# Kernel tuning notes

Measured on AMD Instinct MI355X. Metric: run time of the kernel, lower is better.

## Reference

```python
import jax, jax.numpy as jnp
import numpy as np

IMG = 128                  # img_size
FMM = 35.0
SENSOR = 32.0
FUV = FMM * IMG / SENSOR   # focal length in pixels (screen space, in_ndc=False)
N_PTS = 16384
CHUNK = 1024               # points per scan step
R_SIL = 0.008              # silhouette pass radius (NDC)
R_DEP = 0.012              # depth pass radius (NDC)
K_SIL = 8
K_DEP = 16
DIST = 1.2


def _look_at(dist, elev_deg, azim_deg):
    # PyTorch3D look_at_view_transform with at=origin, up=+Y, degrees=True
    elev = jnp.deg2rad(elev_deg)
    azim = jnp.deg2rad(azim_deg)
    cam = jnp.stack([dist * jnp.cos(elev) * jnp.sin(azim),
                     dist * jnp.sin(elev),
                     dist * jnp.cos(elev) * jnp.cos(azim)], axis=-1)  # (B,3)
    up = jnp.array([0.0, 1.0, 0.0], dtype=cam.dtype)
    z_ax = -cam / (jnp.linalg.norm(cam, axis=-1, keepdims=True) + 1e-8)
    x_ax = jnp.cross(jnp.broadcast_to(up, z_ax.shape), z_ax)
    x_ax = x_ax / (jnp.linalg.norm(x_ax, axis=-1, keepdims=True) + 1e-8)
    y_ax = jnp.cross(z_ax, x_ax)
    R = jnp.stack([x_ax, y_ax, z_ax], axis=-1)   # columns are camera axes
    T = -jnp.einsum('bi,bij->bj', cam, R)        # X_cam = X_world @ R + T
    return R, T


def _project(pts, R, T):
    # world -> camera (row-vector convention) -> screen px -> PyTorch3D NDC
    Xc = jnp.einsum('bni,bij->bnj', pts, R) + T[:, None, :]
    z = Xc[..., 2]
    z_safe = jnp.where(z > 1e-5, z, 1.0)  # points behind camera are culled anyway
    xs = FUV * Xc[..., 0] / z_safe + IMG / 2.0
    ys = FUV * Xc[..., 1] / z_safe + IMG / 2.0
    x_ndc = 1.0 - 2.0 * xs / IMG
    y_ndc = 1.0 - 2.0 * ys / IMG
    return jnp.stack([x_ndc, y_ndc], axis=-1), z


def _rasterize(xy, z, r2, K):
    """Per-pixel K nearest-in-depth points within per-point NDC radius.
    xy: (B,N,2) NDC, z: (B,N) camera depth, r2: (B,N) squared radius.
    Returns zbuf, dists of shape (B,IMG,IMG,K), -1 for empty slots."""
    B, N, _ = xy.shape
    P = IMG * IMG
    # pixel-center NDC grid (PyTorch3D: +X left, +Y up; row-major flatten)
    gxs = 1.0 - (2.0 * jnp.arange(IMG, dtype=xy.dtype) + 1.0) / IMG  # per column
    gys = 1.0 - (2.0 * jnp.arange(IMG, dtype=xy.dtype) + 1.0) / IMG  # per row
    gx = jnp.tile(gxs, IMG)          # (P,)
    gy = jnp.repeat(gys, IMG)        # (P,)

    nch = N // CHUNK
    px = xy[..., 0].reshape(B, nch, CHUNK).swapaxes(0, 1)
    py = xy[..., 1].reshape(B, nch, CHUNK).swapaxes(0, 1)
    pz = z.reshape(B, nch, CHUNK).swapaxes(0, 1)
    pr2 = r2.reshape(B, nch, CHUNK).swapaxes(0, 1)

    def body(carry, c):
        top_z, top_d = carry
        cx, cy, cz, cr2 = c                               # each (B,CHUNK)
        dx = gx[None, :, None] - cx[:, None, :]           # (B,P,CHUNK)
        dy = gy[None, :, None] - cy[:, None, :]
        d2 = dx * dx + dy * dy
        ok = (d2 < cr2[:, None, :]) & (cz[:, None, :] > 0.0)
        zc = jnp.where(ok, cz[:, None, :], jnp.inf)
        cand_z = jnp.concatenate([top_z, zc], axis=-1)    # (B,P,K+CHUNK)
        cand_d = jnp.concatenate([top_d, d2], axis=-1)
        negz, idx = jax.lax.top_k(-cand_z, K)             # K smallest depths
        return (-negz, jnp.take_along_axis(cand_d, idx, axis=-1)), None

    init = (jnp.full((B, P, K), jnp.inf, dtype=xy.dtype),
            jnp.zeros((B, P, K), dtype=xy.dtype))
    (top_z, top_d), _ = jax.lax.scan(jax.checkpoint(body), init, (px, py, pz, pr2))
    valid = jnp.isfinite(top_z)
    zbuf = jnp.where(valid, top_z, -1.0).reshape(B, IMG, IMG, K)
    dists = jnp.where(valid, top_d, -1.0).reshape(B, IMG, IMG, K)
    return zbuf, dists


def setup_inputs() -> dict:
    key = jax.random.key(0)
    k1, k2 = jax.random.split(key)
    point_cloud = jax.random.normal(k1, (2, N_PTS, 6), dtype=jnp.float32) * 0.25
    param = jax.random.normal(k2, (2, 8, 3), dtype=jnp.float32) * 20.0  # degrees
    return {"point_cloud": point_cloud, "param": param}


def reference(point_cloud, param):
    pts = point_cloud[..., :3]
    B = pts.shape[0]
    elev0 = param[:, 1, 0]
    azim0 = param[:, 0, 0]

    # ---- silhouette pass (radius 0.008, K=8) + alpha compositing ----
    R0, T0 = _look_at(DIST, elev0, azim0)
    xy0, z0 = _project(pts, R0, T0)
    r2_sil = jnp.full((B, N_PTS), R_SIL * R_SIL, dtype=pts.dtype)
    _, dists_s = _rasterize(xy0, z0, r2_sil, K_SIL)
    alphas = jnp.where(dists_s >= 0.0, 1.0 - dists_s / (R_SIL * R_SIL), 0.0)
    trans = jnp.cumprod(1.0 - alphas, axis=-1)
    trans_excl = jnp.concatenate([jnp.ones_like(trans[..., :1]), trans[..., :-1]], axis=-1)
    sihlt_map = jnp.sum(alphas * trans_excl, axis=-1, keepdims=True) * 255.0  # (B,H,W,1)

    # ---- depth pass with random view (radius 0.012, K=16) ----
    kd = jax.random.key(42)
    ke, ka = jax.random.split(kd)
    elev_d = jax.random.uniform(ke, (B,), dtype=pts.dtype) * 60.0 - 30.0
    azim_d = jax.random.uniform(ka, (B,), dtype=pts.dtype) * 300.0 + azim0 + 30.0
    Rd, Td = _look_at(DIST, elev_d, azim_d)
    xyd, zd = _project(pts, Rd, Td)
    r2_dep = jnp.full((B, N_PTS), R_DEP * R_DEP, dtype=pts.dtype)
    zbuf_d, _ = _rasterize(xyd, zd, r2_dep, K_DEP)
    depth_ini = zbuf_d[..., 0]

    # density-aware adaptive radius (detached, per source .detach())
    area = jnp.sum((jax.lax.stop_gradient(depth_ini) > 0.0).astype(pts.dtype), axis=(1, 2))
    pa_radius = area / 16384.0 * 0.057                      # (B,)
    r2_ada = jnp.broadcast_to((pa_radius * pa_radius)[:, None], (B, N_PTS))

    zbuf_a, dists_a = _rasterize(xyd, zd, r2_ada, K_DEP)
    depth_img = zbuf_a[..., :8]
    dist_top = dists_a[..., :8]
    return (sihlt_map, depth_img, dist_top)
```

## Files before the change

kernel.cpp:

```cpp
#include <hip/hip_runtime.h>
#include <hip/hip_cooperative_groups.h>
#include <cstring>
#include <cstdint>

namespace cg = cooperative_groups;

#define NPTS 16384
#define FUVC 140.0f
#define R_SILF 0.008f
#define R_DEPF 0.012f
#define R2_SIL (0.008f*0.008f)
#define R2_DEP (0.012f*0.012f)
#define CH 512

#define AREA_OFF  48
#define PA_OFF    50
#define R2ADA_OFF 52
#define CNT_SIL   64
#define OFF_SIL   2112
#define CNT_ADA   4160
#define OFF_ADA   6208
#define FLAGS8    8256
#define FLAGS     8256
#define ZERO_END  16448
#define PROJ0     41024
#define PROJ1     172096
#define LSILF     303168
#define LADAF     827456
#define WS1_WORDS 2007104u
#define WS1_NEEDED ((size_t)WS1_WORDS * 4u)
#define LSIL      303168
#define LADA      434240
#define WS2_WORDS 729152u
#define WS2_NEEDED ((size_t)WS2_WORDS * 4u)

#define FUSED_BLOCKS 1024
#define FUSED_NT (FUSED_BLOCKS * 256)

__device__ __forceinline__ void cam_calc(float elev, float azim, float c[12]) {
    const float D2R = 0.017453292519943295f;
    float er = elev * D2R, ar = azim * D2R;
    float ce = cosf(er), se = sinf(er), ca = cosf(ar), sa = sinf(ar);
    float cx = 1.2f * ce * sa, cy = 1.2f * se, cz = 1.2f * ce * ca;
    float n = sqrtf(cx*cx + cy*cy + cz*cz) + 1e-8f;
    float zx = -cx / n, zy = -cy / n, zz = -cz / n;
    float xx = zz, xy = 0.0f, xz = -zx;
    float xn = sqrtf(xx*xx + xy*xy + xz*xz) + 1e-8f;
    xx /= xn; xz /= xn;
    float yx = zy*xz - zz*xy, yy = zz*xx - zx*xz, yz = zx*xy - zy*xx;
    c[0]=xx; c[1]=xy; c[2]=xz; c[3]=yx; c[4]=yy; c[5]=yz;
    c[6]=zx; c[7]=zy; c[8]=zz;
    c[9]  = -(cx*xx + cy*xy + cz*xz);
    c[10] = -(cx*yx + cy*yy + cz*yz);
    c[11] = -(cx*zx + cy*zy + cz*zz);
}

__device__ __forceinline__ void cam_compute(const float* __restrict__ param,
                                            float* __restrict__ ws,
                                            int t, float ue0, float ue1,
                                            float ua0, float ua1) {
    int b = t >> 1, cam = t & 1;
    float azim0 = param[b * 24 + 0];
    float elev0 = param[b * 24 + 3];
    float elev, azim;
    if (cam == 0) { elev = elev0; azim = azim0; }
    else {
        float ue = b ? ue1 : ue0;
        float ua = b ? ua1 : ua0;
        elev = ue * 60.0f - 30.0f;
        azim = ua * 300.0f + azim0 + 30.0f;
    }
    float c[12];
    cam_calc(elev, azim, c);
    float* w = ws + t * 12;
    #pragma unroll
    for (int i = 0; i < 12; i++) w[i] = c[i];
}

__device__ __forceinline__ float4 project_pt(const float* __restrict__ P,
                                             const float c[12]) {
    float X = P[0], Y = P[1], Z = P[2];
    float xc = X*c[0] + Y*c[1] + Z*c[2] + c[9];
    float yc = X*c[3] + Y*c[4] + Z*c[5] + c[10];
    float zc = X*c[6] + Y*c[7] + Z*c[8] + c[11];
    float zs = zc > 1e-5f ? zc : 1.0f;
    float px = 1.0f - (FUVC * xc / zs + 64.0f) * (1.0f/64.0f);
    float py = 1.0f - (FUVC * yc / zs + 64.0f) * (1.0f/64.0f);
    return make_float4(px, py, zc, 0.0f);
}

__device__ __forceinline__ void pix_range(float p, float r, int& lo, int& hi) {
    float lo_f = (1.0f - p - r) * 64.0f - 0.5f;
    float hi_f = (1.0f - p + r) * 64.0f - 0.5f;
    lo = (int)ceilf(lo_f - 1e-3f);
    hi = (int)floorf(hi_f + 1e-3f);
    lo = max(lo, 0); hi = min(hi, 127);
}

__device__ __forceinline__ void top8_insert(float z, float d,
                                            float tz[8], float td[8]) {
    #pragma unroll
    for (int k = 0; k < 8; k++) {
        bool lt = z < tz[k];
        float oz = tz[k], od = td[k];
        if (lt) { tz[k] = z; td[k] = d; z = oz; d = od; }
    }
}

__device__ __forceinline__ void hit_test(float4 pt, float gx, float gy, float r2,
                                         float tz[8], float td[8]) {
    float dx = gx - pt.x, dy = gy - pt.y;
    float d2 = dx*dx + dy*dy;
    if (d2 < r2 && pt.z > 0.0f && pt.z < tz[7]) top8_insert(pt.z, d2, tz, td);
}

__device__ __forceinline__ void merge_sorted8(float tz[8], float td[8], int mask) {
    float oz[8], od[8];
    #pragma unroll
    for (int k = 0; k < 8; k++) {
        oz[k] = __shfl_xor(tz[k], mask);
        od[k] = __shfl_xor(td[k], mask);
    }
    float mz[8], md[8];
    #pragma unroll
    for (int k = 0; k < 8; k++) {
        bool take = oz[7 - k] < tz[k];
        mz[k] = take ? oz[7 - k] : tz[k];
        md[k] = take ? od[7 - k] : td[k];
    }
    #define CE(i, j) { bool sw = mz[j] < mz[i]; \
        float t1 = mz[i], t2 = md[i]; \
        mz[i] = sw ? mz[j] : mz[i]; md[i] = sw ? md[j] : md[i]; \
        mz[j] = sw ? t1 : mz[j];    md[j] = sw ? t2 : md[j]; }
    CE(0,4) CE(1,5) CE(2,6) CE(3,7)
    CE(0,2) CE(1,3) CE(4,6) CE(5,7)
    CE(0,1) CE(2,3) CE(4,5) CE(6,7)
    #undef CE
    #pragma unroll
    for (int k = 0; k < 8; k++) { tz[k] = mz[k]; td[k] = md[k]; }
}

__device__ __forceinline__ void scan1024(unsigned* uw, unsigned cbase,
                                         unsigned obase, unsigned* s, int t) {
    unsigned c0 = uw[cbase + t*4 + 0];
    unsigned c1 = uw[cbase + t*4 + 1];
    unsigned c2 = uw[cbase + t*4 + 2];
    unsigned c3 = uw[cbase + t*4 + 3];
    unsigned tot = c0 + c1 + c2 + c3;
    s[t] = tot; __syncthreads();
    for (int off = 1; off < 256; off <<= 1) {
        unsigned v = (t >= off) ? s[t - off] : 0u;
        __syncthreads();
        s[t] += v;
        __syncthreads();
    }
    unsigned base = s[t] - tot;
    uw[obase + t*4 + 0] = base;
    uw[obase + t*4 + 1] = base + c0;
    uw[obase + t*4 + 2] = base + c0 + c1;
    uw[obase + t*4 + 3] = base + c0 + c1 + c2;
    uw[cbase + t*4 + 0] = 0;
    uw[cbase + t*4 + 1] = 0;
    uw[cbase + t*4 + 2] = 0;
    uw[cbase + t*4 + 3] = 0;
}

__device__ __forceinline__ void body_proj(const float* __restrict__ pc,
                                          float* __restrict__ ws, int b, int p) {
    unsigned* uw = (unsigned*)ws;
    unsigned char* fb = (unsigned char*)(uw + FLAGS8);
    const float* P = pc + ((size_t)b * NPTS + p) * 6;
    float c0[12], c1[12];
    const float* w0 = ws + (b * 2) * 12;
    #pragma unroll
    for (int i = 0; i < 12; i++) { c0[i] = w0[i]; c1[i] = w0[12 + i]; }

    float4 q0 = project_pt(P, c0);
    ((float4*)(ws + PROJ0))[b * NPTS + p] = q0;
    if (q0.z > 0.0f) {
        int cl, chh, rl, rh;
        pix_range(q0.x, R_SILF, cl, chh);
        pix_range(q0.y, R_SILF, rl, rh);
        if (cl <= chh && rl <= rh) {
            int bxl = cl >> 2, bxh = chh >> 2, byl = rl >> 2, byh = rh >> 2;
            for (int by = byl; by <= byh; by++)
                for (int bx = bxl; bx <= bxh; bx++)
                    atomicAdd(&uw[CNT_SIL + b * 1024 + by * 32 + bx], 1u);
        }
    }

    float4 q1 = project_pt(P, c1);
    ((float4*)(ws + PROJ1))[b * NPTS + p] = q1;
    if (q1.z > 0.0f) {
        int cl, chh, rl, rh;
        pix_range(q1.x, R_DEPF, cl, chh);
        pix_range(q1.y, R_DEPF, rl, rh);
        for (int rr = rl; rr <= rh; rr++) {
            float gy = 1.0f - (float)(2 * rr + 1) * (1.0f/128.0f);
            float dy = gy - q1.y;
            for (int cc = cl; cc <= chh; cc++) {
                float gx = 1.0f - (float)(2 * cc + 1) * (1.0f/128.0f);
                float dx = gx - q1.x;
                float d2 = dx*dx + dy*dy;
                if (d2 < R2_DEP) fb[b * NPTS + rr * 128 + cc] = 1;
            }
        }
    }
}

__device__ __forceinline__ void body_area_scan(float* __restrict__ ws, int job,
                                               int t, unsigned* s) {
    unsigned* uw = (unsigned*)ws;
    if (job < 2) {
        int b = job;
        unsigned acc = 0;
        #pragma unroll
        for (int j = 0; j < 16; j++) {
            unsigned w = uw[FLAGS8 + b * 4096 + t * 16 + j];
            acc += __popc(w & 0x01010101u);
        }
        s[t] = acc; __syncthreads();
        for (int off = 128; off > 0; off >>= 1) {
            if (t < off) s[t] += s[t + off];
            __syncthreads();
        }
        if (t == 0) {
            unsigned area = s[0];
            uw[AREA_OFF + b] = area;
            float pa = (float)area * (1.0f/16384.0f) * 0.057f;
            ws[PA_OFF + b] = pa;
            ws[R2ADA_OFF + b] = pa * pa;
        }
    } else {
        int b = job - 2;
        scan1024(uw, CNT_SIL + b * 1024, OFF_SIL + b * 1024, s, t);
    }
}

__device__ __forceinline__ void body_cnt_ada(float* __restrict__ ws, int p) {
    unsigned* uw = (unsigned*)ws;
    int b = p >> 14;
    float4 q = ((const float4*)(ws + PROJ1))[p];
    float pa = ws[PA_OFF + b];
    if (q.z > 0.0f) {
        int cl, chh, rl, rh;
        pix_range(q.x, pa, cl, chh);
        pix_range(q.y, pa, rl, rh);
        if (cl <= chh && rl <= rh) {
            int bxl = cl >> 2, bxh = chh >> 2, byl = rl >> 2, byh = rh >> 2;
            for (int by = byl; by <= byh; by++)
                for (int bx = bxl; bx <= bxh; bx++)
                    atomicAdd(&uw[CNT_ADA + b * 1024 + by * 32 + bx], 1u);
        }
    }
}

__device__ __forceinline__ void body_scat_sil(float* __restrict__ ws, int p) {
    unsigned* uw = (unsigned*)ws;
    int b = p >> 14;
    float4 q = ((const float4*)(ws + PROJ0))[p];
    if (q.z > 0.0f) {
        int cl, chh, rl, rh;
        pix_range(q.x, R_SILF, cl, chh);
        pix_range(q.y, R_SILF, rl, rh);
        if (cl <= chh && rl <= rh) {
            int bxl = cl >> 2, bxh = chh >> 2, byl = rl >> 2, byh = rh >> 2;
            for (int by = byl; by <= byh; by++)
                for (int bx = bxl; bx <= bxh; bx++) {
                    unsigned bin = b * 1024 + by * 32 + bx;
                    unsigned idx = uw[OFF_SIL + bin] + atomicAdd(&uw[CNT_SIL + bin], 1u);
                    ((float4*)(ws + LSILF))[b * 65536 + idx] = q;
                }
        }
    }
}

__device__ __forceinline__ void body_scan_ada(float* __restrict__ ws, int b, int t) {
    unsigned* uw = (unsigned*)ws;
    unsigned c[16]; unsigned tot = 0;
    #pragma unroll
    for (int j = 0; j < 16; j++) { c[j] = uw[CNT_ADA + b * 1024 + t * 16 + j]; tot += c[j]; }
    unsigned inc = tot;
    #pragma unroll
    for (int off = 1; off < 64; off <<= 1) {
        unsigned v = __shfl_up(inc, off);
        if (t >= off) inc += v;
    }
    unsigned base = inc - tot;
    #pragma unroll
    for (int j = 0; j < 16; j++) {
        uw[OFF_ADA + b * 1024 + t * 16 + j] = base;
        base += c[j];
        uw[CNT_ADA + b * 1024 + t * 16 + j] = 0u;
    }
}

__device__ __forceinline__ void body_scat_ada(float* __restrict__ ws, int p) {
    unsigned* uw = (unsigned*)ws;
    int b = p >> 14;
    float4 q = ((const float4*)(ws + PROJ1))[p];
    float pa = ws[PA_OFF + b];
    if (q.z > 0.0f) {
        int cl, chh, rl, rh;
        pix_range(q.x, pa, cl, chh);
        pix_range(q.y, pa, rl, rh);
        if (cl <= chh && rl <= rh) {
            int bxl = cl >> 2, bxh = chh >> 2, byl = rl >> 2, byh = rh >> 2;
            for (int by = byl; by <= byh; by++)
                for (int bx = bxl; bx <= bxh; bx++) {
                    unsigned bin = b * 1024 + by * 32 + bx;
                    unsigned idx = uw[OFF_ADA + bin] + atomicAdd(&uw[CNT_ADA + bin], 1u);
                    ((float4*)(ws + LADAF))[b * 147456 + idx] = q;
                }
        }
    }
}

__device__ __forceinline__ void body_gather(const float* __restrict__ ws,
                                            float* __restrict__ out,
                                            int id, int lane) {
    const unsigned* uw = (const unsigned*)ws;
    bool sil = id < 2048;
    int gt = sil ? id : id - 2048;
    int b = gt >> 10;
    int tile = gt & 1023;
    int p = lane & 15, s = lane >> 4;
    int bx = tile & 31, by = tile >> 5;
    int col = (bx << 2) + (p & 3), row = (by << 2) + (p >> 2);
    float gx = 1.0f - (float)(2*col + 1) * (1.0f/128.0f);
    float gy = 1.0f - (float)(2*row + 1) * (1.0f/128.0f);
    float r2 = sil ? R2_SIL : ws[R2ADA_OFF + b];
    unsigned start = sil ? uw[OFF_SIL + b * 1024 + tile] : uw[OFF_ADA + b * 1024 + tile];
    unsigned len   = sil ? uw[CNT_SIL + b * 1024 + tile] : uw[CNT_ADA + b * 1024 + tile];
    const float4* lst = sil ? ((const float4*)(ws + LSILF)) + b * 65536 + start
                            : ((const float4*)(ws + LADAF)) + b * 147456 + start;

    float tz[8], td[8];
    #pragma unroll
    for (int k = 0; k < 8; k++) { tz[k] = INFINITY; td[k] = 0.0f; }

    unsigned i = (unsigned)s;
    while (i + 28 < len) {
        float4 cb[8];
        #pragma unroll
        for (int u = 0; u < 8; u++) cb[u] = lst[i + 4u * (unsigned)u];
        #pragma unroll
        for (int u = 0; u < 8; u++) hit_test(cb[u], gx, gy, r2, tz, td);
        i += 32;
    }
    for (; i < len; i += 4) hit_test(lst[i], gx, gy, r2, tz, td);

    merge_sorted8(tz, td, 16);
    merge_sorted8(tz, td, 32);

    if (s == 0) {
        int pix = (b << 14) + row * 128 + col;
        if (sil) {
            float trans = 1.0f, acc = 0.0f;
            #pragma unroll
            for (int k = 0; k < 8; k++) {
                float a = (tz[k] != INFINITY) ? (1.0f - td[k] / R2_SIL) : 0.0f;
                acc += a * trans;
                trans *= (1.0f - a);
            }
            out[pix] = acc * 255.0f;
        } else {
            float* dep = out + 32768  + (size_t)pix * 8;
            float* dst = out + 294912 + (size_t)pix * 8;
            #pragma unroll
            for (int k = 0; k < 8; k++) {
                bool v = (tz[k] != INFINITY);
                dep[k] = v ? tz[k] : -1.0f;
                dst[k] = v ? td[k] : -1.0f;
            }
        }
    }
}

__global__ __launch_bounds__(256) void k_fused(const float* __restrict__ pc,
                                               const float* __restrict__ param,
                                               float* __restrict__ ws,
                                               float* __restrict__ out,
                                               float ue0, float ue1,
                                               float ua0, float ua1) {
    cg::grid_group grid = cg::this_grid();
    unsigned* uw = (unsigned*)ws;
    __shared__ unsigned s[256];
    int tid = blockIdx.x * 256 + threadIdx.x;

    for (int i = 48 + tid; i < ZERO_END; i += FUSED_NT) uw[i] = 0u;
    if (tid < 4) cam_compute(param, ws, tid, ue0, ue1, ua0, ua1);
    grid.sync();

    if (tid < 2 * NPTS) body_proj(pc, ws, tid >> 14, tid & (NPTS - 1));
    grid.sync();

    if (blockIdx.x < 4) body_area_scan(ws, blockIdx.x, threadIdx.x, s);
    grid.sync();

    if (tid < 2 * NPTS) body_cnt_ada(ws, tid);
    else if (tid < 4 * NPTS) body_scat_sil(ws, tid - 2 * NPTS);
    grid.sync();

    if (blockIdx.x == 0 && threadIdx.x < 128)
        body_scan_ada(ws, threadIdx.x >> 6, threadIdx.x & 63);
    grid.sync();

    if (tid < 2 * NPTS) body_scat_ada(ws, tid);
    grid.sync();

    body_gather(ws, out, tid >> 6, tid & 63);
}


__global__ __launch_bounds__(256) void k_zero(float* __restrict__ ws) {
    unsigned* uw = (unsigned*)ws;
    int gid = blockIdx.x * 256 + threadIdx.x;
    int stride = gridDim.x * 256;
    for (int i = gid; i < ZERO_END; i += stride) uw[i] = 0u;
}

__global__ __launch_bounds__(256) void k_proj_v3(const float* __restrict__ pc,
                                                 const float* __restrict__ param,
                                                 float* __restrict__ ws,
                                                 float ue0, float ue1,
                                                 float ua0, float ua1) {
    int b = blockIdx.x >> 6;
    int p = ((blockIdx.x & 63) << 8) + threadIdx.x;
    float azim0 = param[b * 24 + 0];
    float elev0 = param[b * 24 + 3];
    float c0[12], c1[12];
    cam_calc(elev0, azim0, c0);
    float ue = b ? ue1 : ue0;
    float ua = b ? ua1 : ua0;
    cam_calc(ue * 60.0f - 30.0f, ua * 300.0f + azim0 + 30.0f, c1);

    unsigned* uw = (unsigned*)ws;
    unsigned char* fb = (unsigned char*)(uw + FLAGS8);
    const float* P = pc + ((size_t)b * NPTS + p) * 6;

    float4 q0 = project_pt(P, c0);
    ((float4*)(ws + PROJ0))[b * NPTS + p] = q0;
    if (q0.z > 0.0f) {
        int cl, chh, rl, rh;
        pix_range(q0.x, R_SILF, cl, chh);
        pix_range(q0.y, R_SILF, rl, rh);
        if (cl <= chh && rl <= rh) {
            int bxl = cl >> 2, bxh = chh >> 2, byl = rl >> 2, byh = rh >> 2;
            for (int by = byl; by <= byh; by++)
                for (int bx = bxl; bx <= bxh; bx++)
                    atomicAdd(&uw[CNT_SIL + b * 1024 + by * 32 + bx], 1u);
        }
    }
    float4 q1 = project_pt(P, c1);
    ((float4*)(ws + PROJ1))[b * NPTS + p] = q1;
    if (q1.z > 0.0f) {
        int cl, chh, rl, rh;
        pix_range(q1.x, R_DEPF, cl, chh);
        pix_range(q1.y, R_DEPF, rl, rh);
        for (int rr = rl; rr <= rh; rr++) {
            float gy = 1.0f - (float)(2 * rr + 1) * (1.0f/128.0f);
            float dy = gy - q1.y;
            for (int cc = cl; cc <= chh; cc++) {
                float gx = 1.0f - (float)(2 * cc + 1) * (1.0f/128.0f);
                float dx = gx - q1.x;
                float d2 = dx*dx + dy*dy;
                if (d2 < R2_DEP) fb[b * NPTS + rr * 128 + cc] = 1;
            }
        }
    }
}

__global__ __launch_bounds__(256) void k_area_scan_v3(float* __restrict__ ws) {
    __shared__ unsigned s[256];
    body_area_scan(ws, blockIdx.x, threadIdx.x, s);
}

__global__ __launch_bounds__(64) void k_cntada_scatsil(float* __restrict__ ws) {
    int id = blockIdx.x;
    bool isCnt = id < 512;
    int p = ((isCnt ? id : id - 512) << 6) + threadIdx.x;
    if (isCnt) body_cnt_ada(ws, p);
    else       body_scat_sil(ws, p);
}

__global__ __launch_bounds__(64) void k_scan_ada64(float* __restrict__ ws) {
    body_scan_ada(ws, blockIdx.x, threadIdx.x);
}

__global__ __launch_bounds__(64) void k_scatter_ada_v2(float* __restrict__ ws) {
    body_scat_ada(ws, (blockIdx.x << 6) + threadIdx.x);
}

__global__ __launch_bounds__(64) void k_gather_v3(const float* __restrict__ ws,
                                                  float* __restrict__ out) {
    body_gather(ws, out, blockIdx.x, threadIdx.x);
}


__global__ __launch_bounds__(256) void k_init(const float* __restrict__ param,
                                              float* __restrict__ ws,
                                              float ue0, float ue1,
                                              float ua0, float ua1) {
    unsigned* uw = (unsigned*)ws;
    int gid = blockIdx.x * 256 + threadIdx.x;
    int stride = gridDim.x * 256;
    for (int i = gid; i < 2048; i += stride) { uw[CNT_SIL + i] = 0u; uw[CNT_ADA + i] = 0u; }
    for (int i = gid; i < 32768; i += stride) uw[FLAGS + i] = 0u;
    if (gid < 2) uw[AREA_OFF + gid] = 0u;
    if (gid < 4) cam_compute(param, ws, gid, ue0, ue1, ua0, ua1);
}

__global__ __launch_bounds__(256) void k_proj_count(const float* __restrict__ pc,
                                                    float* __restrict__ ws) {
    unsigned* uw = (unsigned*)ws;
    int b = blockIdx.x >> 6;
    int p = ((blockIdx.x & 63) << 8) + threadIdx.x;
    const float* P = pc + ((size_t)b * NPTS + p) * 6;
    float c0[12], c1[12];
    const float* w0 = ws + (b * 2) * 12;
    #pragma unroll
    for (int i = 0; i < 12; i++) { c0[i] = w0[i]; c1[i] = w0[12 + i]; }

    float4 q0 = project_pt(P, c0);
    ((float4*)(ws + PROJ0))[b * NPTS + p] = q0;
    if (q0.z > 0.0f) {
        int cl, chh, rl, rh;
        pix_range(q0.x, R_SILF, cl, chh);
        pix_range(q0.y, R_SILF, rl, rh);
        if (cl <= chh && rl <= rh) {
            int bxl = cl >> 2, bxh = chh >> 2, byl = rl >> 2, byh = rh >> 2;
            for (int by = byl; by <= byh; by++)
                for (int bx = bxl; bx <= bxh; bx++)
                    atomicAdd(&uw[CNT_SIL + b * 1024 + by * 32 + bx], 1u);
        }
    }
    float4 q1 = project_pt(P, c1);
    ((float4*)(ws + PROJ1))[b * NPTS + p] = q1;
    if (q1.z > 0.0f) {
        int cl, chh, rl, rh;
        pix_range(q1.x, R_DEPF, cl, chh);
        pix_range(q1.y, R_DEPF, rl, rh);
        for (int rr = rl; rr <= rh; rr++) {
            float gy = 1.0f - (float)(2 * rr + 1) * (1.0f/128.0f);
            float dy = gy - q1.y;
            for (int cc = cl; cc <= chh; cc++) {
                float gx = 1.0f - (float)(2 * cc + 1) * (1.0f/128.0f);
                float dx = gx - q1.x;
                float d2 = dx*dx + dy*dy;
                if (d2 < R2_DEP) uw[FLAGS + b * NPTS + rr * 128 + cc] = 1u;
            }
        }
    }
}

__global__ __launch_bounds__(256) void k_area_scan(float* __restrict__ ws) {
    unsigned* uw = (unsigned*)ws;
    __shared__ unsigned s[256];
    int t = threadIdx.x;
    int job = blockIdx.x;
    if (job < 2) {
        int b = job;
        unsigned acc = 0;
        for (int i = t; i < NPTS; i += 256) acc += uw[FLAGS + b * NPTS + i];
        s[t] = acc; __syncthreads();
        for (int off = 128; off > 0; off >>= 1) {
            if (t < off) s[t] += s[t + off];
            __syncthreads();
        }
        if (t == 0) {
            unsigned area = s[0];
            uw[AREA_OFF + b] = area;
            float pa = (float)area * (1.0f/16384.0f) * 0.057f;
            ws[PA_OFF + b] = pa;
            ws[R2ADA_OFF + b] = pa * pa;
        }
    } else {
        int b = job - 2;
        scan1024(uw, CNT_SIL + b * 1024, OFF_SIL + b * 1024, s, t);
    }
}

__global__ __launch_bounds__(256) void k_count_ada(float* __restrict__ ws) {
    unsigned* uw = (unsigned*)ws;
    int b = blockIdx.x >> 6;
    int p = ((blockIdx.x & 63) << 8) + threadIdx.x;
    float4 q = ((const float4*)(ws + PROJ1))[b * NPTS + p];
    float pa = ws[PA_OFF + b];
    if (q.z > 0.0f) {
        int cl, chh, rl, rh;
        pix_range(q.x, pa, cl, chh);
        pix_range(q.y, pa, rl, rh);
        if (cl <= chh && rl <= rh) {
            int bxl = cl >> 2, bxh = chh >> 2, byl = rl >> 2, byh = rh >> 2;
            for (int by = byl; by <= byh; by++)
                for (int bx = bxl; bx <= bxh; bx++)
                    atomicAdd(&uw[CNT_ADA + b * 1024 + by * 32 + bx], 1u);
        }
    }
}

__global__ __launch_bounds__(256) void k_scan_ada(float* __restrict__ ws) {
    unsigned* uw = (unsigned*)ws;
    __shared__ unsigned s[256];
    int b = blockIdx.x;
    scan1024(uw, CNT_ADA + b * 1024, OFF_ADA + b * 1024, s, threadIdx.x);
}

__global__ __launch_bounds__(256) void k_scatter(float* __restrict__ ws) {
    unsigned* uw = (unsigned*)ws;
    int b = blockIdx.x >> 6;
    int p = ((blockIdx.x & 63) << 8) + threadIdx.x;

    float4 q0 = ((const float4*)(ws + PROJ0))[b * NPTS + p];
    if (q0.z > 0.0f) {
        int cl, chh, rl, rh;
        pix_range(q0.x, R_SILF, cl, chh);
        pix_range(q0.y, R_SILF, rl, rh);
        if (cl <= chh && rl <= rh) {
            int bxl = cl >> 2, bxh = chh >> 2, byl = rl >> 2, byh = rh >> 2;
            for (int by = byl; by <= byh; by++)
                for (int bx = bxl; bx <= bxh; bx++) {
                    unsigned bin = b * 1024 + by * 32 + bx;
                    unsigned idx = uw[OFF_SIL + bin] + atomicAdd(&uw[CNT_SIL + bin], 1u);
                    uw[LSIL + b * 65536 + idx] = (unsigned)p;
                }
        }
    }
    float4 q1 = ((const float4*)(ws + PROJ1))[b * NPTS + p];
    float pa = ws[PA_OFF + b];
    if (q1.z > 0.0f) {
        int cl, chh, rl, rh;
        pix_range(q1.x, pa, cl, chh);
        pix_range(q1.y, pa, rl, rh);
        if (cl <= chh && rl <= rh) {
            int bxl = cl >> 2, bxh = chh >> 2, byl = rl >> 2, byh = rh >> 2;
            for (int by = byl; by <= byh; by++)
                for (int bx = bxl; bx <= bxh; bx++) {
                    unsigned bin = b * 1024 + by * 32 + bx;
                    unsigned idx = uw[OFF_ADA + bin] + atomicAdd(&uw[CNT_ADA + bin], 1u);
                    uw[LADA + b * 147456 + idx] = (unsigned)p;
                }
        }
    }
}

__global__ __launch_bounds__(256) void k_gather_sil(const float* __restrict__ ws,
                                                    float* __restrict__ out) {
    const unsigned* uw = (const unsigned*)ws;
    int b = blockIdx.x >> 6;
    int tile = (blockIdx.x & 63) * 16 + (threadIdx.x >> 4);
    int q = threadIdx.x & 15;
    int bx = tile & 31, by = tile >> 5;
    int col = (bx << 2) + (q & 3), row = (by << 2) + (q >> 2);
    float gx = 1.0f - (float)(2*col + 1) * (1.0f/128.0f);
    float gy = 1.0f - (float)(2*row + 1) * (1.0f/128.0f);
    unsigned start = uw[OFF_SIL + b * 1024 + tile];
    unsigned len   = uw[CNT_SIL + b * 1024 + tile];
    const float4* pr = (const float4*)(ws + PROJ0) + b * NPTS;

    float tz[8], td[8];
    #pragma unroll
    for (int k = 0; k < 8; k++) { tz[k] = INFINITY; td[k] = 0.0f; }
    for (unsigned i = 0; i < len; i++) {
        unsigned pid = uw[LSIL + b * 65536 + start + i];
        hit_test(pr[pid], gx, gy, R2_SIL, tz, td);
    }
    float trans = 1.0f, s = 0.0f;
    #pragma unroll
    for (int k = 0; k < 8; k++) {
        float a = (tz[k] != INFINITY) ? (1.0f - td[k] / R2_SIL) : 0.0f;
        s += a * trans;
        trans *= (1.0f - a);
    }
    out[(b << 14) + row * 128 + col] = s * 255.0f;
}

__global__ __launch_bounds__(256) void k_gather_ada(const float* __restrict__ ws,
                                                    float* __restrict__ out) {
    const unsigned* uw = (const unsigned*)ws;
    int b = blockIdx.x >> 6;
    int tile = (blockIdx.x & 63) * 16 + (threadIdx.x >> 4);
    int q = threadIdx.x & 15;
    int bx = tile & 31, by = tile >> 5;
    int col = (bx << 2) + (q & 3), row = (by << 2) + (q >> 2);
    float gx = 1.0f - (float)(2*col + 1) * (1.0f/128.0f);
    float gy = 1.0f - (float)(2*row + 1) * (1.0f/128.0f);
    float r2 = ws[R2ADA_OFF + b];
    unsigned start = uw[OFF_ADA + b * 1024 + tile];
    unsigned len   = uw[CNT_ADA + b * 1024 + tile];
    const float4* pr = (const float4*)(ws + PROJ1) + b * NPTS;

    float tz[8], td[8];
    #pragma unroll
    for (int k = 0; k < 8; k++) { tz[k] = INFINITY; td[k] = 0.0f; }
    for (unsigned i = 0; i < len; i++) {
        unsigned pid = uw[LADA + b * 147456 + start + i];
        hit_test(pr[pid], gx, gy, r2, tz, td);
    }
    int pix = (b << 14) + row * 128 + col;
    float* dep = out + 32768  + (size_t)pix * 8;
    float* dst = out + 294912 + (size_t)pix * 8;
    #pragma unroll
    for (int k = 0; k < 8; k++) {
        bool v = (tz[k] != INFINITY);
        dep[k] = v ? tz[k] : -1.0f;
        dst[k] = v ? td[k] : -1.0f;
    }
}

__global__ void cam_kernel_fb(const float* __restrict__ param, float* __restrict__ ws,
                              float ue0, float ue1, float ua0, float ua1) {
    int t = threadIdx.x;
    if (t < 2) ws[48 + t] = 0.0f;
    if (t >= 4) return;
    cam_compute(param, ws, t, ue0, ue1, ua0, ua1);
}

__device__ __forceinline__ void stage_points(const float* __restrict__ pcb,
                                             const float c[12], int c0, float4* sp) {
    for (int i = threadIdx.x; i < CH; i += 256) {
        const float* P = pcb + (size_t)(c0 + i) * 6;
        sp[i] = project_pt(P, c);
    }
}

__global__ __launch_bounds__(256) void raster_AB(const float* __restrict__ pc,
                                                 float* __restrict__ ws,
                                                 float* __restrict__ out) {
    __shared__ float4 sp[CH];
    int bid = blockIdx.x;
    bool silMode = bid < 128;
    int q = silMode ? bid : bid - 128;
    int b = q >> 6;
    int p = ((q & 63) << 8) + threadIdx.x;
    const float* cw = ws + (b * 2 + (silMode ? 0 : 1)) * 12;
    float c[12];
    #pragma unroll
    for (int i = 0; i < 12; i++) c[i] = cw[i];
    float r2 = silMode ? R2_SIL : R2_DEP;
    int col = p & 127, row = p >> 7;
    float gx = 1.0f - (float)(2*col + 1) * (1.0f/128.0f);
    float gy = 1.0f - (float)(2*row + 1) * (1.0f/128.0f);
    const float* pcb = pc + (size_t)b * NPTS * 6;

    if (silMode) {
        float tz[8], td[8];
        #pragma unroll
        for (int k = 0; k < 8; k++) { tz[k] = INFINITY; td[k] = 0.0f; }
        for (int c0 = 0; c0 < NPTS; c0 += CH) {
            __syncthreads();
            stage_points(pcb, c, c0, sp);
            __syncthreads();
            #pragma unroll 4
            for (int j = 0; j < CH; j++) hit_test(sp[j], gx, gy, r2, tz, td);
        }
        float trans = 1.0f, s = 0.0f;
        #pragma unroll
        for (int k = 0; k < 8; k++) {
            float a = (tz[k] != INFINITY) ? (1.0f - td[k] / r2) : 0.0f;
            s += a * trans;
            trans *= (1.0f - a);
        }
        out[(b << 14) + p] = s * 255.0f;
    } else {
        float mz = INFINITY;
        for (int c0 = 0; c0 < NPTS; c0 += CH) {
            __syncthreads();
            stage_points(pcb, c, c0, sp);
            __syncthreads();
            #pragma unroll 4
            for (int j = 0; j < CH; j++) {
                float4 pt = sp[j];
                float dx = gx - pt.x, dy = gy - pt.y;
                float d2 = dx*dx + dy*dy;
                if (d2 < r2 && pt.z > 0.0f) mz = fminf(mz, pt.z);
            }
        }
        unsigned long long m = __ballot(mz != INFINITY);
        if ((threadIdx.x & 63) == 0)
            atomicAdd(ws + 48 + b, (float)__popcll(m));
    }
}

__global__ __launch_bounds__(256) void raster_C(const float* __restrict__ pc,
                                                const float* __restrict__ ws,
                                                float* __restrict__ out) {
    __shared__ float4 sp[CH];
    int bid = blockIdx.x;
    int b = bid >> 6;
    int p = ((bid & 63) << 8) + threadIdx.x;
    const float* cw = ws + (b * 2 + 1) * 12;
    float c[12];
    #pragma unroll
    for (int i = 0; i < 12; i++) c[i] = cw[i];
    float area = ws[48 + b];
    float pa = (area * (1.0f/16384.0f)) * 0.057f;
    float r2 = pa * pa;
    int col = p & 127, row = p >> 7;
    float gx = 1.0f - (float)(2*col + 1) * (1.0f/128.0f);
    float gy = 1.0f - (float)(2*row + 1) * (1.0f/128.0f);
    const float* pcb = pc + (size_t)b * NPTS * 6;

    float tz[8], td[8];
    #pragma unroll
    for (int k = 0; k < 8; k++) { tz[k] = INFINITY; td[k] = 0.0f; }
    for (int c0 = 0; c0 < NPTS; c0 += CH) {
        __syncthreads();
        stage_points(pcb, c, c0, sp);
        __syncthreads();
        #pragma unroll 4
        for (int j = 0; j < CH; j++) hit_test(sp[j], gx, gy, r2, tz, td);
    }
    float* dep = out + 32768  + (size_t)((b << 14) + p) * 8;
    float* dst = out + 294912 + (size_t)((b << 14) + p) * 8;
    #pragma unroll
    for (int k = 0; k < 8; k++) {
        bool v = (tz[k] != INFINITY);
        dep[k] = v ? tz[k] : -1.0f;
        dst[k] = v ? td[k] : -1.0f;
    }
}

static inline uint32_t rotl32(uint32_t x, int r) { return (x << r) | (x >> (32 - r)); }

static void tf2x32(uint32_t k0, uint32_t k1, uint32_t c0, uint32_t c1,
                   uint32_t* o0, uint32_t* o1) {
    uint32_t ks0 = k0, ks1 = k1, ks2 = k0 ^ k1 ^ 0x1BD11BDAu;
    uint32_t x0 = c0 + ks0, x1 = c1 + ks1;
    static const int rA[4] = {13, 15, 26, 6};
    static const int rB[4] = {17, 29, 16, 24};
    #define RND4(R) do { for (int i = 0; i < 4; i++) { x0 += x1; x1 = rotl32(x1, R[i]); x1 ^= x0; } } while (0)
    RND4(rA); x0 += ks1; x1 += ks2 + 1u;
    RND4(rB); x0 += ks2; x1 += ks0 + 2u;
    RND4(rA); x0 += ks0; x1 += ks1 + 3u;
    RND4(rB); x0 += ks1; x1 += ks2 + 4u;
    RND4(rA); x0 += ks2; x1 += ks0 + 5u;
    #undef RND4
    *o0 = x0; *o1 = x1;
}

static inline float bits_to_unit_float(uint32_t bits) {
    uint32_t fb = (bits >> 9) | 0x3f800000u;
    float f;
    memcpy(&f, &fb, 4);
    return f - 1.0f;
}

extern "C" void kernel_launch(void* const* d_in, const int* in_sizes, int n_in,
                              void* d_out, int out_size, void* d_ws, size_t ws_size,
                              hipStream_t stream) {
    const float* pc    = (const float*)d_in[0];
    const float* param = (const float*)d_in[1];
    float* out = (float*)d_out;
    float* ws  = (float*)d_ws;

    uint32_t ke0, ke1, ka0, ka1, b1, b2;
    tf2x32(0u, 42u, 0u, 0u, &ke0, &ke1);
    tf2x32(0u, 42u, 0u, 1u, &ka0, &ka1);
    float ue[2], ua[2];
    for (uint32_t i = 0; i < 2; i++) {
        tf2x32(ke0, ke1, 0u, i, &b1, &b2);
        ue[i] = bits_to_unit_float(b1 ^ b2);
        tf2x32(ka0, ka1, 0u, i, &b1, &b2);
        ua[i] = bits_to_unit_float(b1 ^ b2);
    }
    float ue0 = ue[0], ue1 = ue[1], ua0 = ua[0], ua1 = ua[1];

    if (ws_size >= WS1_NEEDED) {
        int dev = 0;
        hipGetDevice(&dev);
        hipDeviceProp_t prop;
        bool coop = (hipGetDeviceProperties(&prop, dev) == hipSuccess) &&
                    prop.cooperativeLaunch;
        if (coop) {
            int maxB = 0;
            if (hipOccupancyMaxActiveBlocksPerMultiprocessor(&maxB, k_fused, 256, 0)
                    != hipSuccess ||
                maxB * prop.multiProcessorCount < FUSED_BLOCKS)
                coop = false;
        }
        if (coop) {
            void* args[] = { (void*)&pc, (void*)&param, (void*)&ws, (void*)&out,
                             (void*)&ue0, (void*)&ue1, (void*)&ua0, (void*)&ua1 };
            hipError_t e = hipLaunchCooperativeKernel((const void*)k_fused,
                                                      dim3(FUSED_BLOCKS), dim3(256),
                                                      args, 0, stream);
            if (e == hipSuccess) return;
        }
        k_zero          <<<16, 256, 0, stream>>>(ws);
        k_proj_v3       <<<128, 256, 0, stream>>>(pc, param, ws, ue0, ue1, ua0, ua1);
        k_area_scan_v3  <<<4, 256, 0, stream>>>(ws);
        k_cntada_scatsil<<<1024, 64, 0, stream>>>(ws);
        k_scan_ada64    <<<2, 64, 0, stream>>>(ws);
        k_scatter_ada_v2<<<512, 64, 0, stream>>>(ws);
        k_gather_v3     <<<4096, 64, 0, stream>>>(ws, out);
    } else if (ws_size >= WS2_NEEDED) {
        k_init      <<<64, 256, 0, stream>>>(param, ws, ue0, ue1, ua0, ua1);
        k_proj_count<<<128, 256, 0, stream>>>(pc, ws);
        k_area_scan <<<4, 256, 0, stream>>>(ws);
        k_count_ada <<<128, 256, 0, stream>>>(ws);
        k_scan_ada  <<<2, 256, 0, stream>>>(ws);
        k_scatter   <<<128, 256, 0, stream>>>(ws);
        k_gather_sil<<<128, 256, 0, stream>>>(ws, out);
        k_gather_ada<<<128, 256, 0, stream>>>(ws, out);
    } else {
        cam_kernel_fb<<<1, 64, 0, stream>>>(param, ws, ue0, ue1, ua0, ua1);
        raster_AB<<<256, 256, 0, stream>>>(pc, ws, out);
        raster_C <<<128, 256, 0, stream>>>(pc, ws, out);
    }
}
```

Baseline: 92.22 us.

## Cut grid syncs via last-block tickets and aggregate bin atomics in shared memory

The cooperative fused kernel drops two of its grid-wide barriers. Small serial steps (area/scan, ada scan) now run in whichever block finishes last, detected with a global atomic ticket counter. Each block first builds its per-bin counts and scatter offsets in a shared-memory histogram and then issues one global atomic per bin, instead of one global atomic per point per bin. This lowers global atomic contention and barrier latency, but adds extra __syncthreads, threadfences and shared-memory work, and changes the scatter order within a bin.

Measured after the change: 92.52 us. No clear change (+0.3%).

```diff
diff --git a/kernel.cpp b/kernel.cpp
--- a/kernel.cpp
+++ b/kernel.cpp
@@ -16,6 +16,8 @@
 #define AREA_OFF  48
 #define PA_OFF    50
 #define R2ADA_OFF 52
+#define TICK0     54
+#define TICK1     55
 #define CNT_SIL   64
 #define OFF_SIL   2112
 #define CNT_ADA   4160
@@ -97,6 +99,19 @@
     lo = max(lo, 0); hi = min(hi, 127);
 }
 
+__device__ __forceinline__ void bin_bbox(float4 q, float r, int& bxl, int& bxh,
+                                         int& byl, int& byh) {
+    bxl = 0; bxh = -1; byl = 0; byh = -1;
+    if (q.z > 0.0f) {
+        int cl, chh, rl, rh;
+        pix_range(q.x, r, cl, chh);
+        pix_range(q.y, r, rl, rh);
+        if (cl <= chh && rl <= rh) {
+            bxl = cl >> 2; bxh = chh >> 2; byl = rl >> 2; byh = rh >> 2;
+        }
+    }
+}
+
 __device__ __forceinline__ void top8_insert(float z, float d,
                                             float tz[8], float td[8]) {
     #pragma unroll
@@ -165,49 +180,6 @@
     uw[cbase + t*4 + 3] = 0;
 }
 
-__device__ __forceinline__ void body_proj(const float* __restrict__ pc,
-                                          float* __restrict__ ws, int b, int p) {
-    unsigned* uw = (unsigned*)ws;
-    unsigned char* fb = (unsigned char*)(uw + FLAGS8);
-    const float* P = pc + ((size_t)b * NPTS + p) * 6;
-    float c0[12], c1[12];
-    const float* w0 = ws + (b * 2) * 12;
-    #pragma unroll
-    for (int i = 0; i < 12; i++) { c0[i] = w0[i]; c1[i] = w0[12 + i]; }
-
-    float4 q0 = project_pt(P, c0);
-    ((float4*)(ws + PROJ0))[b * NPTS + p] = q0;
-    if (q0.z > 0.0f) {
-        int cl, chh, rl, rh;
-        pix_range(q0.x, R_SILF, cl, chh);
-        pix_range(q0.y, R_SILF, rl, rh);
-        if (cl <= chh && rl <= rh) {
-            int bxl = cl >> 2, bxh = chh >> 2, byl = rl >> 2, byh = rh >> 2;
-            for (int by = byl; by <= byh; by++)
-                for (int bx = bxl; bx <= bxh; bx++)
-                    atomicAdd(&uw[CNT_SIL + b * 1024 + by * 32 + bx], 1u);
-        }
-    }
-
-    float4 q1 = project_pt(P, c1);
-    ((float4*)(ws + PROJ1))[b * NPTS + p] = q1;
-    if (q1.z > 0.0f) {
-        int cl, chh, rl, rh;
-        pix_range(q1.x, R_DEPF, cl, chh);
-        pix_range(q1.y, R_DEPF, rl, rh);
-        for (int rr = rl; rr <= rh; rr++) {
-            float gy = 1.0f - (float)(2 * rr + 1) * (1.0f/128.0f);
-            float dy = gy - q1.y;
-            for (int cc = cl; cc <= chh; cc++) {
-                float gx = 1.0f - (float)(2 * cc + 1) * (1.0f/128.0f);
-                float dx = gx - q1.x;
-                float d2 = dx*dx + dy*dy;
-                if (d2 < R2_DEP) fb[b * NPTS + rr * 128 + cc] = 1;
-            }
-        }
-    }
-}
-
 __device__ __forceinline__ void body_area_scan(float* __restrict__ ws, int job,
                                                int t, unsigned* s) {
     unsigned* uw = (unsigned*)ws;
@@ -242,37 +214,25 @@
     int b = p >> 14;
     float4 q = ((const float4*)(ws + PROJ1))[p];
     float pa = ws[PA_OFF + b];
-    if (q.z > 0.0f) {
-        int cl, chh, rl, rh;
-        pix_range(q.x, pa, cl, chh);
-        pix_range(q.y, pa, rl, rh);
-        if (cl <= chh && rl <= rh) {
-            int bxl = cl >> 2, bxh = chh >> 2, byl = rl >> 2, byh = rh >> 2;
-            for (int by = byl; by <= byh; by++)
-                for (int bx = bxl; bx <= bxh; bx++)
-                    atomicAdd(&uw[CNT_ADA + b * 1024 + by * 32 + bx], 1u);
-        }
-    }
+    int bxl, bxh, byl, byh;
+    bin_bbox(q, pa, bxl, bxh, byl, byh);
+    for (int by = byl; by <= byh; by++)
+        for (int bx = bxl; bx <= bxh; bx++)
+            atomicAdd(&uw[CNT_ADA + b * 1024 + by * 32 + bx], 1u);
 }
 
 __device__ __forceinline__ void body_scat_sil(float* __restrict__ ws, int p) {
     unsigned* uw = (unsigned*)ws;
     int b = p >> 14;
     float4 q = ((const float4*)(ws + PROJ0))[p];
-    if (q.z > 0.0f) {
-        int cl, chh, rl, rh;
-        pix_range(q.x, R_SILF, cl, chh);
-        pix_range(q.y, R_SILF, rl, rh);
-        if (cl <= chh && rl <= rh) {
-            int bxl = cl >> 2, bxh = chh >> 2, byl = rl >> 2, byh = rh >> 2;
-            for (int by = byl; by <= byh; by++)
-                for (int bx = bxl; bx <= bxh; bx++) {
-                    unsigned bin = b * 1024 + by * 32 + bx;
-                    unsigned idx = uw[OFF_SIL + bin] + atomicAdd(&uw[CNT_SIL + bin], 1u);
-                    ((float4*)(ws + LSILF))[b * 65536 + idx] = q;
-                }
-        }
-    }
+    int bxl, bxh, byl, byh;
+    bin_bbox(q, R_SILF, bxl, bxh, byl, byh);
+    for (int by = byl; by <= byh; by++)
+        for (int bx = bxl; bx <= bxh; bx++) {
+            unsigned bin = b * 1024 + by * 32 + bx;
+            unsigned idx = uw[OFF_SIL + bin] + atomicAdd(&uw[CNT_SIL + bin], 1u);
+            ((float4*)(ws + LSILF))[b * 65536 + idx] = q;
+        }
 }
 
 __device__ __forceinline__ void body_scan_ada(float* __restrict__ ws, int b, int t) {
@@ -300,20 +260,14 @@
     int b = p >> 14;
     float4 q = ((const float4*)(ws + PROJ1))[p];
     float pa = ws[PA_OFF + b];
-    if (q.z > 0.0f) {
-        int cl, chh, rl, rh;
-        pix_range(q.x, pa, cl, chh);
-        pix_range(q.y, pa, rl, rh);
-        if (cl <= chh && rl <= rh) {
-            int bxl = cl >> 2, bxh = chh >> 2, byl = rl >> 2, byh = rh >> 2;
-            for (int by = byl; by <= byh; by++)
-                for (int bx = bxl; bx <= bxh; bx++) {
-                    unsigned bin = b * 1024 + by * 32 + bx;
-                    unsigned idx = uw[OFF_ADA + bin] + atomicAdd(&uw[CNT_ADA + bin], 1u);
-                    ((float4*)(ws + LADAF))[b * 147456 + idx] = q;
-                }
-        }
-    }
+    int bxl, bxh, byl, byh;
+    bin_bbox(q, pa, bxl, bxh, byl, byh);
+    for (int by = byl; by <= byh; by++)
+        for (int bx = bxl; bx <= bxh; bx++) {
+            unsigned bin = b * 1024 + by * 32 + bx;
+            unsigned idx = uw[OFF_ADA + bin] + atomicAdd(&uw[CNT_ADA + bin], 1u);
+            ((float4*)(ws + LADAF))[b * 147456 + idx] = q;
+        }
 }
 
 __device__ __forceinline__ void body_gather(const float* __restrict__ ws,
@@ -377,36 +331,175 @@
     }
 }
 
-__global__ __launch_bounds__(256) void k_fused(const float* __restrict__ pc,
-                                               const float* __restrict__ param,
-                                               float* __restrict__ ws,
-                                               float* __restrict__ out,
-                                               float ue0, float ue1,
-                                               float ua0, float ua1) {
+__global__ __launch_bounds__(256) void k_fusedp(const float* __restrict__ pc,
+                                                const float* __restrict__ param,
+                                                float* __restrict__ ws,
+                                                float* __restrict__ out,
+                                                float ue0, float ue1,
+                                                float ua0, float ua1) {
     cg::grid_group grid = cg::this_grid();
     unsigned* uw = (unsigned*)ws;
-    __shared__ unsigned s[256];
-    int tid = blockIdx.x * 256 + threadIdx.x;
+    __shared__ unsigned sh[2048];
+    __shared__ unsigned shLast;
+    int t = threadIdx.x;
+    int tid = blockIdx.x * 256 + t;
 
     for (int i = 48 + tid; i < ZERO_END; i += FUSED_NT) uw[i] = 0u;
     if (tid < 4) cam_compute(param, ws, tid, ue0, ue1, ua0, ua1);
     grid.sync();
 
-    if (tid < 2 * NPTS) body_proj(pc, ws, tid >> 14, tid & (NPTS - 1));
+    if (blockIdx.x < 128) {
+        int b = blockIdx.x >> 6;
+        int p = ((blockIdx.x & 63) << 8) + t;
+        unsigned char* fb = (unsigned char*)(uw + FLAGS8);
+        const float* P = pc + ((size_t)b * NPTS + p) * 6;
+        float c0[12], c1[12];
+        const float* w0 = ws + (b * 2) * 12;
+        #pragma unroll
+        for (int i = 0; i < 12; i++) { c0[i] = w0[i]; c1[i] = w0[12 + i]; }
+
+        #pragma unroll
+        for (int j = 0; j < 4; j++) sh[t * 4 + j] = 0u;
+        __syncthreads();
+
+        float4 q0 = project_pt(P, c0);
+        ((float4*)(ws + PROJ0))[b * NPTS + p] = q0;
+        int bxl, bxh, byl, byh;
+        bin_bbox(q0, R_SILF, bxl, bxh, byl, byh);
+        for (int by = byl; by <= byh; by++)
+            for (int bx = bxl; bx <= bxh; bx++)
+                atomicAdd(&sh[by * 32 + bx], 1u);
+
+        float4 q1 = project_pt(P, c1);
+        ((float4*)(ws + PROJ1))[b * NPTS + p] = q1;
+        if (q1.z > 0.0f) {
+            int cl, chh, rl, rh;
+            pix_range(q1.x, R_DEPF, cl, chh);
+            pix_range(q1.y, R_DEPF, rl, rh);
+            for (int rr = rl; rr <= rh; rr++) {
+                float gyv = 1.0f - (float)(2 * rr + 1) * (1.0f/128.0f);
+                float dy = gyv - q1.y;
+                for (int cc = cl; cc <= chh; cc++) {
+                    float gxv = 1.0f - (float)(2 * cc + 1) * (1.0f/128.0f);
+                    float dx = gxv - q1.x;
+                    if (dx*dx + dy*dy < R2_DEP) fb[b * NPTS + rr * 128 + cc] = 1;
+                }
+            }
+        }
+        __syncthreads();
+        #pragma unroll
+        for (int j = 0; j < 4; j++) {
+            unsigned c = sh[t * 4 + j];
+            if (c) atomicAdd(&uw[CNT_SIL + b * 1024 + t * 4 + j], c);
+        }
+        __threadfence();
+    }
+    if (t == 0) shLast = (atomicAdd(&uw[TICK0], 1u) == FUSED_BLOCKS - 1) ? 1u : 0u;
+    __syncthreads();
+    if (shLast) {
+        __threadfence();
+        for (int job = 0; job < 4; job++) {
+            body_area_scan(ws, job, t, sh);
+            __syncthreads();
+        }
+        __threadfence();
+    }
     grid.sync();
 
-    if (blockIdx.x < 4) body_area_scan(ws, blockIdx.x, threadIdx.x, s);
+    if (blockIdx.x < 128) {
+        int b = blockIdx.x >> 6;
+        int p = ((blockIdx.x & 63) << 8) + t;
+        float4 q = ((const float4*)(ws + PROJ1))[b * NPTS + p];
+        float pa = ws[PA_OFF + b];
+        #pragma unroll
+        for (int j = 0; j < 4; j++) sh[t * 4 + j] = 0u;
+        __syncthreads();
+        int bxl, bxh, byl, byh;
+        bin_bbox(q, pa, bxl, bxh, byl, byh);
+        for (int by = byl; by <= byh; by++)
+            for (int bx = bxl; bx <= bxh; bx++)
+                atomicAdd(&sh[by * 32 + bx], 1u);
+        __syncthreads();
+        #pragma unroll
+        for (int j = 0; j < 4; j++) {
+            unsigned c = sh[t * 4 + j];
+            if (c) atomicAdd(&uw[CNT_ADA + b * 1024 + t * 4 + j], c);
+        }
+        __threadfence();
+    } else if (blockIdx.x < 256) {
+        int blk = blockIdx.x - 128;
+        int b = blk >> 6;
+        int p = ((blk & 63) << 8) + t;
+        float4 q = ((const float4*)(ws + PROJ0))[b * NPTS + p];
+        int bxl, bxh, byl, byh;
+        bin_bbox(q, R_SILF, bxl, bxh, byl, byh);
+        #pragma unroll
+        for (int j = 0; j < 4; j++) sh[t * 4 + j] = 0u;
+        __syncthreads();
+        for (int by = byl; by <= byh; by++)
+            for (int bx = bxl; bx <= bxh; bx++)
+                atomicAdd(&sh[by * 32 + bx], 1u);
+        __syncthreads();
+        #pragma unroll
+        for (int j = 0; j < 4; j++) {
+            int bin = t * 4 + j;
+            unsigned c = sh[bin];
+            unsigned gb = 0;
+            if (c) gb = uw[OFF_SIL + b * 1024 + bin] +
+                        atomicAdd(&uw[CNT_SIL + b * 1024 + bin], c);
+            sh[1024 + bin] = gb;
+            sh[bin] = 0u;
+        }
+        __syncthreads();
+        for (int by = byl; by <= byh; by++)
+            for (int bx = bxl; bx <= bxh; bx++) {
+                int bin = by * 32 + bx;
+                unsigned loc = atomicAdd(&sh[bin], 1u);
+                ((float4*)(ws + LSILF))[b * 65536 + sh[1024 + bin] + loc] = q;
+            }
+        __threadfence();
+    }
+    if (t == 0) shLast = (atomicAdd(&uw[TICK1], 1u) == FUSED_BLOCKS - 1) ? 1u : 0u;
+    __syncthreads();
+    if (shLast) {
+        __threadfence();
+        if (t < 128) body_scan_ada(ws, t >> 6, t & 63);
+        __threadfence();
+    }
     grid.sync();
 
-    if (tid < 2 * NPTS) body_cnt_ada(ws, tid);
-    else if (tid < 4 * NPTS) body_scat_sil(ws, tid - 2 * NPTS);
-    grid.sync();
-
-    if (blockIdx.x == 0 && threadIdx.x < 128)
-        body_scan_ada(ws, threadIdx.x >> 6, threadIdx.x & 63);
-    grid.sync();
-
-    if (tid < 2 * NPTS) body_scat_ada(ws, tid);
+    if (blockIdx.x < 128) {
+        int b = blockIdx.x >> 6;
+        int p = ((blockIdx.x & 63) << 8) + t;
+        float4 q = ((const float4*)(ws + PROJ1))[b * NPTS + p];
+        float pa = ws[PA_OFF + b];
+        int bxl, bxh, byl, byh;
+        bin_bbox(q, pa, bxl, bxh, byl, byh);
+        #pragma unroll
+        for (int j = 0; j < 4; j++) sh[t * 4 + j] = 0u;
+        __syncthreads();
+        for (int by = byl; by <= byh; by++)
+            for (int bx = bxl; bx <= bxh; bx++)
+                atomicAdd(&sh[by * 32 + bx], 1u);
+        __syncthreads();
+        #pragma unroll
+        for (int j = 0; j < 4; j++) {
+            int bin = t * 4 + j;
+            unsigned c = sh[bin];
+            unsigned gb = 0;
+            if (c) gb = uw[OFF_ADA + b * 1024 + bin] +
+                        atomicAdd(&uw[CNT_ADA + b * 1024 + bin], c);
+            sh[1024 + bin] = gb;
+            sh[bin] = 0u;
+        }
+        __syncthreads();
+        for (int by = byl; by <= byh; by++)
+            for (int bx = bxl; bx <= bxh; bx++) {
+                int bin = by * 32 + bx;
+                unsigned loc = atomicAdd(&sh[bin], 1u);
+                ((float4*)(ws + LADAF))[b * 147456 + sh[1024 + bin] + loc] = q;
+            }
+    }
     grid.sync();
 
     body_gather(ws, out, tid >> 6, tid & 63);
@@ -417,7 +510,7 @@
     unsigned* uw = (unsigned*)ws;
     int gid = blockIdx.x * 256 + threadIdx.x;
     int stride = gridDim.x * 256;
-    for (int i = gid; i < ZERO_END; i += stride) uw[i] = 0u;
+    for (int i = 48 + gid; i < ZERO_END; i += stride) uw[i] = 0u;
 }
 
 __global__ __launch_bounds__(256) void k_proj_v3(const float* __restrict__ pc,
@@ -441,17 +534,12 @@
 
     float4 q0 = project_pt(P, c0);
     ((float4*)(ws + PROJ0))[b * NPTS + p] = q0;
-    if (q0.z > 0.0f) {
-        int cl, chh, rl, rh;
-        pix_range(q0.x, R_SILF, cl, chh);
-        pix_range(q0.y, R_SILF, rl, rh);
-        if (cl <= chh && rl <= rh) {
-            int bxl = cl >> 2, bxh = chh >> 2, byl = rl >> 2, byh = rh >> 2;
-            for (int by = byl; by <= byh; by++)
-                for (int bx = bxl; bx <= bxh; bx++)
-                    atomicAdd(&uw[CNT_SIL + b * 1024 + by * 32 + bx], 1u);
-        }
-    }
+    int bxl, bxh, byl, byh;
+    bin_bbox(q0, R_SILF, bxl, bxh, byl, byh);
+    for (int by = byl; by <= byh; by++)
+        for (int bx = bxl; bx <= bxh; bx++)
+            atomicAdd(&uw[CNT_SIL + b * 1024 + by * 32 + bx], 1u);
+
     float4 q1 = project_pt(P, c1);
     ((float4*)(ws + PROJ1))[b * NPTS + p] = q1;
     if (q1.z > 0.0f) {
@@ -464,8 +552,7 @@
             for (int cc = cl; cc <= chh; cc++) {
                 float gx = 1.0f - (float)(2 * cc + 1) * (1.0f/128.0f);
                 float dx = gx - q1.x;
-                float d2 = dx*dx + dy*dy;
-                if (d2 < R2_DEP) fb[b * NPTS + rr * 128 + cc] = 1;
+                if (dx*dx + dy*dy < R2_DEP) fb[b * NPTS + rr * 128 + cc] = 1;
             }
         }
     }
@@ -524,17 +611,12 @@
 
     float4 q0 = project_pt(P, c0);
     ((float4*)(ws + PROJ0))[b * NPTS + p] = q0;
-    if (q0.z > 0.0f) {
-        int cl, chh, rl, rh;
-        pix_range(q0.x, R_SILF, cl, chh);
-        pix_range(q0.y, R_SILF, rl, rh);
-        if (cl <= chh && rl <= rh) {
-            int bxl = cl >> 2, bxh = chh >> 2, byl = rl >> 2, byh = rh >> 2;
-            for (int by = byl; by <= byh; by++)
-                for (int bx = bxl; bx <= bxh; bx++)
-                    atomicAdd(&uw[CNT_SIL + b * 1024 + by * 32 + bx], 1u);
-        }
-    }
+    int bxl, bxh, byl, byh;
+    bin_bbox(q0, R_SILF, bxl, bxh, byl, byh);
+    for (int by = byl; by <= byh; by++)
+        for (int bx = bxl; bx <= bxh; bx++)
+            atomicAdd(&uw[CNT_SIL + b * 1024 + by * 32 + bx], 1u);
+
     float4 q1 = project_pt(P, c1);
     ((float4*)(ws + PROJ1))[b * NPTS + p] = q1;
     if (q1.z > 0.0f) {
@@ -547,8 +629,7 @@
             for (int cc = cl; cc <= chh; cc++) {
                 float gx = 1.0f - (float)(2 * cc + 1) * (1.0f/128.0f);
                 float dx = gx - q1.x;
-                float d2 = dx*dx + dy*dy;
-                if (d2 < R2_DEP) uw[FLAGS + b * NPTS + rr * 128 + cc] = 1u;
+                if (dx*dx + dy*dy < R2_DEP) uw[FLAGS + b * NPTS + rr * 128 + cc] = 1u;
             }
         }
     }
@@ -582,22 +663,9 @@
 }
 
 __global__ __launch_bounds__(256) void k_count_ada(float* __restrict__ ws) {
-    unsigned* uw = (unsigned*)ws;
     int b = blockIdx.x >> 6;
     int p = ((blockIdx.x & 63) << 8) + threadIdx.x;
-    float4 q = ((const float4*)(ws + PROJ1))[b * NPTS + p];
-    float pa = ws[PA_OFF + b];
-    if (q.z > 0.0f) {
-        int cl, chh, rl, rh;
-        pix_range(q.x, pa, cl, chh);
-        pix_range(q.y, pa, rl, rh);
-        if (cl <= chh && rl <= rh) {
-            int bxl = cl >> 2, bxh = chh >> 2, byl = rl >> 2, byh = rh >> 2;
-            for (int by = byl; by <= byh; by++)
-                for (int bx = bxl; bx <= bxh; bx++)
-                    atomicAdd(&uw[CNT_ADA + b * 1024 + by * 32 + bx], 1u);
-        }
-    }
+    body_cnt_ada(ws, b * NPTS + p);
 }
 
 __global__ __launch_bounds__(256) void k_scan_ada(float* __restrict__ ws) {
@@ -613,36 +681,24 @@
     int p = ((blockIdx.x & 63) << 8) + threadIdx.x;
 
     float4 q0 = ((const float4*)(ws + PROJ0))[b * NPTS + p];
-    if (q0.z > 0.0f) {
-        int cl, chh, rl, rh;
-        pix_range(q0.x, R_SILF, cl, chh);
-        pix_range(q0.y, R_SILF, rl, rh);
-        if (cl <= chh && rl <= rh) {
-            int bxl = cl >> 2, bxh = chh >> 2, byl = rl >> 2, byh = rh >> 2;
-            for (int by = byl; by <= byh; by++)
-                for (int bx = bxl; bx <= bxh; bx++) {
-                    unsigned bin = b * 1024 + by * 32 + bx;
-                    unsigned idx = uw[OFF_SIL + bin] + atomicAdd(&uw[CNT_SIL + bin], 1u);
-                    uw[LSIL + b * 65536 + idx] = (unsigned)p;
-                }
-        }
-    }
+    int bxl, bxh, byl, byh;
+    bin_bbox(q0, R_SILF, bxl, bxh, byl, byh);
+    for (int by = byl; by <= byh; by++)
+        for (int bx = bxl; bx <= bxh; bx++) {
+            unsigned bin = b * 1024 + by * 32 + bx;
+            unsigned idx = uw[OFF_SIL + bin] + atomicAdd(&uw[CNT_SIL + bin], 1u);
+            uw[LSIL + b * 65536 + idx] = (unsigned)p;
+        }
+
     float4 q1 = ((const float4*)(ws + PROJ1))[b * NPTS + p];
     float pa = ws[PA_OFF + b];
-    if (q1.z > 0.0f) {
-        int cl, chh, rl, rh;
-        pix_range(q1.x, pa, cl, chh);
-        pix_range(q1.y, pa, rl, rh);
-        if (cl <= chh && rl <= rh) {
-            int bxl = cl >> 2, bxh = chh >> 2, byl = rl >> 2, byh = rh >> 2;
-            for (int by = byl; by <= byh; by++)
-                for (int bx = bxl; bx <= bxh; bx++) {
-                    unsigned bin = b * 1024 + by * 32 + bx;
-                    unsigned idx = uw[OFF_ADA + bin] + atomicAdd(&uw[CNT_ADA + bin], 1u);
-                    uw[LADA + b * 147456 + idx] = (unsigned)p;
-                }
-        }
-    }
+    bin_bbox(q1, pa, bxl, bxh, byl, byh);
+    for (int by = byl; by <= byh; by++)
+        for (int bx = bxl; bx <= bxh; bx++) {
+            unsigned bin = b * 1024 + by * 32 + bx;
+            unsigned idx = uw[OFF_ADA + bin] + atomicAdd(&uw[CNT_ADA + bin], 1u);
+            uw[LADA + b * 147456 + idx] = (unsigned)p;
+        }
 }
 
 __global__ __launch_bounds__(256) void k_gather_sil(const float* __restrict__ ws,
@@ -875,7 +931,7 @@
                     prop.cooperativeLaunch;
         if (coop) {
             int maxB = 0;
-            if (hipOccupancyMaxActiveBlocksPerMultiprocessor(&maxB, k_fused, 256, 0)
+            if (hipOccupancyMaxActiveBlocksPerMultiprocessor(&maxB, k_fusedp, 256, 0)
                     != hipSuccess ||
                 maxB * prop.multiProcessorCount < FUSED_BLOCKS)
                 coop = false;
@@ -883,7 +939,7 @@
         if (coop) {
             void* args[] = { (void*)&pc, (void*)&param, (void*)&ws, (void*)&out,
                              (void*)&ue0, (void*)&ue1, (void*)&ua0, (void*)&ua1 };
-            hipError_t e = hipLaunchCooperativeKernel((const void*)k_fused,
+            hipError_t e = hipLaunchCooperativeKernel((const void*)k_fusedp,
                                                       dim3(FUSED_BLOCKS), dim3(256),
                                                       args, 0, stream);
             if (e == hipSuccess) return;
```
